# Kernel optimization log

Hardware: AMD Instinct MI355X
Metric: run time of the kernel (lower is better)

The kernel has to match this reference:

```python
import jax, jax.numpy as jnp
import numpy as np

D_MODEL = 1024
N_HEADS = 16
HEAD_DIM = D_MODEL // N_HEADS
D_FF = 4096
ROPE_BASE = 10000.0
LN_EPS = 1e-5


def setup_inputs() -> dict:
    key = jax.random.key(0)
    ks = jax.random.split(key, 12)
    B, S = 2, 2048
    s = 0.02
    inp = {
        "x": jax.random.normal(ks[0], (B, S, D_MODEL), dtype=jnp.float32),
        "Wq": jax.random.normal(ks[1], (D_MODEL, D_MODEL), dtype=jnp.float32) * s,
        "bq": jnp.zeros((D_MODEL,), jnp.float32),
        "Wk": jax.random.normal(ks[2], (D_MODEL, D_MODEL), dtype=jnp.float32) * s,
        "bk": jnp.zeros((D_MODEL,), jnp.float32),
        "Wv": jax.random.normal(ks[3], (D_MODEL, D_MODEL), dtype=jnp.float32) * s,
        "bv": jnp.zeros((D_MODEL,), jnp.float32),
        "Wo": jax.random.normal(ks[4], (D_MODEL, D_MODEL), dtype=jnp.float32) * s,
        "bo": jnp.zeros((D_MODEL,), jnp.float32),
        "ln1_g": jnp.ones((D_MODEL,), jnp.float32),
        "ln1_b": jnp.zeros((D_MODEL,), jnp.float32),
        "W1": jax.random.normal(ks[5], (D_MODEL, D_FF), dtype=jnp.float32) * s,
        "b1": jnp.zeros((D_FF,), jnp.float32),
        "W2": jax.random.normal(ks[6], (D_FF, D_MODEL), dtype=jnp.float32) * s,
        "b2": jnp.zeros((D_MODEL,), jnp.float32),
        "ln2_g": jnp.ones((D_MODEL,), jnp.float32),
        "ln2_b": jnp.zeros((D_MODEL,), jnp.float32),
    }
    return inp


def _layernorm(x, g, b):
    mu = jnp.mean(x, axis=-1, keepdims=True)
    var = jnp.var(x, axis=-1, keepdims=True)
    return (x - mu) * jax.lax.rsqrt(var + LN_EPS) * g + b


def _rope_cos_sin(seq_len, dtype):
    inv_freq = 1.0 / (ROPE_BASE ** (jnp.arange(0, HEAD_DIM, 2, dtype=jnp.float32) / HEAD_DIM))
    t = jnp.arange(seq_len, dtype=jnp.float32)
    freqs = jnp.einsum("i,j->ij", t, inv_freq)          # [S, HEAD_DIM/2]
    emb = jnp.concatenate([freqs, freqs], axis=-1)        # [S, HEAD_DIM]
    return jnp.cos(emb).astype(dtype), jnp.sin(emb).astype(dtype)


def _rotate_half(x):
    x1, x2 = jnp.split(x, 2, axis=-1)
    return jnp.concatenate([-x2, x1], axis=-1)


def reference(x, Wq, bq, Wk, bk, Wv, bv, Wo, bo, ln1_g, ln1_b,
              W1, b1, W2, b2, ln2_g, ln2_b):
    B, S, _ = x.shape
    residual = x
    h = _layernorm(x, ln1_g, ln1_b)

    def split_heads(y):  # [B,S,D] -> [B,H,S,hd]
        return y.reshape(B, S, N_HEADS, HEAD_DIM).transpose(0, 2, 1, 3)

    q = split_heads(h @ Wq + bq)
    k = split_heads(h @ Wk + bk)
    v = split_heads(h @ Wv + bv)

    cos, sin = _rope_cos_sin(S, x.dtype)  # [S, hd], broadcast over B,H
    q = q * cos + _rotate_half(q) * sin
    k = k * cos + _rotate_half(k) * sin

    scale = HEAD_DIM ** -0.5
    scores = jnp.einsum("bhqd,bhkd->bhqk", q, k) * scale
    attn = jax.nn.softmax(scores, axis=-1)
    ctx = jnp.einsum("bhqk,bhkd->bhqd", attn, v)           # [B,H,S,hd]
    ctx = ctx.transpose(0, 2, 1, 3).reshape(B, S, D_MODEL)
    attn_out = ctx @ Wo + bo

    x = residual + attn_out
    residual = x
    h = _layernorm(x, ln2_g, ln2_b)
    ffn = jax.nn.gelu(h @ W1 + b1, approximate=False) @ W2 + b2
    return residual + ffn
```

## Files before the change

### kernel.cpp

```cpp
#include <hip/hip_runtime.h>
#include <hip/hip_bf16.h>
#include <stdint.h>

#define S_LEN 2048
#define NH 16
#define HD 64
#define DM 1024
#define DFF 4096
#define MTOK 4096

typedef __attribute__((ext_vector_type(8))) short short8;
typedef __attribute__((ext_vector_type(4))) float f32x4;
typedef __attribute__((ext_vector_type(16))) float f32x16;
typedef __attribute__((ext_vector_type(2))) int i32x2;
typedef unsigned short u16;
typedef unsigned int u32;

__device__ __forceinline__ float bf2f(u16 u) {
  union { u32 i; float f; } x; x.i = ((u32)u) << 16; return x.f;
}
__device__ __forceinline__ u16 f2bf(float f) {
  union { float f; u32 i; } x; x.f = f;
  u32 r = x.i + 0x7fffu + ((x.i >> 16) & 1u);
  return (u16)(r >> 16);
}
__device__ __forceinline__ void gload16(const u16* g, u16* l) {
  __builtin_amdgcn_global_load_lds(
      (__attribute__((address_space(1))) u32*)g,
      (__attribute__((address_space(3))) u32*)l, 16, 0, 0);
}

#define VM0 asm volatile("s_waitcnt vmcnt(0)" ::: "memory")
#define VM6 asm volatile("s_waitcnt vmcnt(6)" ::: "memory")
#define BARR do { __builtin_amdgcn_s_barrier(); asm volatile("" ::: "memory"); } while (0)
#define LGKM0 do { asm volatile("s_waitcnt lgkmcnt(0)" ::: "memory"); __builtin_amdgcn_sched_barrier(0); } while (0)
#define PRIO1 __builtin_amdgcn_s_setprio(1)
#define PRIO0 __builtin_amdgcn_s_setprio(0)

__device__ __forceinline__ void transpose_tile(const float* __restrict__ W,
                                               u16* __restrict__ Wt, int K, int N,
                                               int n0, int k0, int tx, int ty,
                                               float (*tile)[33]) {
#pragma unroll
  for (int i = 0; i < 4; ++i)
    tile[ty + i * 8][tx] = W[(size_t)(k0 + ty + i * 8) * N + n0 + tx];
  __syncthreads();
#pragma unroll
  for (int i = 0; i < 4; ++i)
    Wt[(size_t)(n0 + ty + i * 8) * K + k0 + tx] = f2bf(tile[tx][ty + i * 8]);
}

__global__ __launch_bounds__(256) void prep(
    const float* __restrict__ Wq, const float* __restrict__ Wk,
    const float* __restrict__ Wv, const float* __restrict__ Wo,
    const float* __restrict__ W1, const float* __restrict__ W2,
    u16* __restrict__ WQKVT, u16* __restrict__ WOT, u16* __restrict__ W1T,
    u16* __restrict__ W2T, float* __restrict__ cosT, float* __restrict__ sinT,
    const float* __restrict__ x, const float* __restrict__ g,
    const float* __restrict__ b, u16* __restrict__ H) {
  __shared__ float tile[32][33];
  __shared__ float red[8];
  const int r = blockIdx.x;
  const int t = threadIdx.x;
  const int tx = t & 31, ty = t >> 5;
  if (r < 4096) {
    const float* W = (r < 1024) ? Wq : (r < 2048) ? Wk : (r < 3072) ? Wv : Wo;
    u16* Wt = (r < 1024) ? WQKVT
              : (r < 2048) ? WQKVT + 1024 * 1024
              : (r < 3072) ? WQKVT + 2 * 1024 * 1024 : WOT;
    int sub = r & 1023;
    transpose_tile(W, Wt, 1024, 1024, (sub & 31) * 32, (sub >> 5) * 32, tx, ty, tile);
  } else if (r < 8192) {
    int sub = r - 4096;
    transpose_tile(W1, W1T, 1024, 4096, (sub & 127) * 32, (sub >> 7) * 32, tx, ty, tile);
  } else if (r < 12288) {
    int sub = r - 8192;
    transpose_tile(W2, W2T, 4096, 1024, (sub & 31) * 32, (sub >> 5) * 32, tx, ty, tile);
  } else if (r < 12544) {
    int id = (r - 12288) * 256 + t;
    int s = id >> 5, j = id & 31;
    float inv = powf(10000.0f, -(float)j * (1.0f / 32.0f));
    float fr = (float)s * inv;
    cosT[id] = cosf(fr);
    sinT[id] = sinf(fr);
  } else {
    int row = r - 12544;
    float4 v = ((const float4*)(x + ((size_t)row << 10)))[t];
    float s = v.x + v.y + v.z + v.w;
    float q = v.x * v.x + v.y * v.y + v.z * v.z + v.w * v.w;
#pragma unroll
    for (int m = 1; m < 64; m <<= 1) {
      s += __shfl_xor(s, m, 64);
      q += __shfl_xor(q, m, 64);
    }
    int lane = t & 63, w = t >> 6;
    if (lane == 0) { red[w] = s; red[4 + w] = q; }
    __syncthreads();
    s = red[0] + red[1] + red[2] + red[3];
    q = red[4] + red[5] + red[6] + red[7];
    float mu = s * (1.0f / 1024.0f);
    float var = q * (1.0f / 1024.0f) - mu * mu;
    float rstd = rsqrtf(var + 1e-5f);
    float4 gv = ((const float4*)g)[t];
    float4 bv = ((const float4*)b)[t];
    ushort4 o;
    o.x = f2bf((v.x - mu) * rstd * gv.x + bv.x);
    o.y = f2bf((v.y - mu) * rstd * gv.y + bv.y);
    o.z = f2bf((v.z - mu) * rstd * gv.z + bv.z);
    o.w = f2bf((v.w - mu) * rstd * gv.w + bv.w);
    ((ushort4*)(H + ((size_t)row << 10)))[t] = o;
  }
}

__global__ __launch_bounds__(256) void ln_bf16(const float* __restrict__ x,
                                               const float* __restrict__ g,
                                               const float* __restrict__ b,
                                               u16* __restrict__ out) {
  int row = blockIdx.x;
  int t = threadIdx.x;
  float4 v = ((const float4*)(x + ((size_t)row << 10)))[t];
  float s = v.x + v.y + v.z + v.w;
  float q = v.x * v.x + v.y * v.y + v.z * v.z + v.w * v.w;
#pragma unroll
  for (int m = 1; m < 64; m <<= 1) {
    s += __shfl_xor(s, m, 64);
    q += __shfl_xor(q, m, 64);
  }
  __shared__ float red[8];
  int lane = t & 63, w = t >> 6;
  if (lane == 0) { red[w] = s; red[4 + w] = q; }
  __syncthreads();
  s = red[0] + red[1] + red[2] + red[3];
  q = red[4] + red[5] + red[6] + red[7];
  float mu = s * (1.0f / 1024.0f);
  float var = q * (1.0f / 1024.0f) - mu * mu;
  float rstd = rsqrtf(var + 1e-5f);
  float4 gv = ((const float4*)g)[t];
  float4 bv = ((const float4*)b)[t];
  ushort4 o;
  o.x = f2bf((v.x - mu) * rstd * gv.x + bv.x);
  o.y = f2bf((v.y - mu) * rstd * gv.y + bv.y);
  o.z = f2bf((v.z - mu) * rstd * gv.z + bv.z);
  o.w = f2bf((v.w - mu) * rstd * gv.w + bv.w);
  ((ushort4*)(out + ((size_t)row << 10)))[t] = o;
}

#define MMQ(IB, NB)                                                          \
  _Pragma("unroll") for (int i_ = 0; i_ < 4; ++i_)                           \
  _Pragma("unroll") for (int n_ = 0; n_ < 2; ++n_)                           \
  _Pragma("unroll") for (int k_ = 0; k_ < 2; ++k_)                           \
    acc[(IB) + i_][(NB) + n_] = __builtin_amdgcn_mfma_f32_16x16x32_bf16(     \
        a[i_][k_], b[(NB) + n_][k_], acc[(IB) + i_][(NB) + n_], 0, 0, 0);

template <int EPI>
__global__ __launch_bounds__(512, 2) void gemm256(
    const u16* __restrict__ A, const u16* __restrict__ Bt, int N, int K,
    const float* __restrict__ bias, const float* __restrict__ bq,
    const float* __restrict__ bk, const float* __restrict__ bv,
    const float* __restrict__ cosT, const float* __restrict__ sinT,
    u16* __restrict__ d0, u16* __restrict__ d1, u16* __restrict__ d2) {
  __shared__ __align__(16) u16 As[2][256 * 64];
  __shared__ __align__(16) u16 Bs[2][256 * 64];
  const int t = threadIdx.x;
  const int lane = t & 63, wid = t >> 6;
  const int fr = lane & 15, fq = lane >> 4;
  const int m0 = blockIdx.y << 8, n0 = blockIdx.x << 8;
  const int wmo = (wid >> 2) << 7;
  const int wno = (wid & 3) << 6;
  const int r7 = fr & 7;
  const int srow = t >> 3, ssl = t & 7;

  f32x4 acc[8][4];
#pragma unroll
  for (int i = 0; i < 8; ++i)
#pragma unroll
    for (int n = 0; n < 4; ++n) acc[i][n] = (f32x4){0.f, 0.f, 0.f, 0.f};

  short8 a[4][2], b[4][2];

  auto stageA = [&](int slot, int kt) {
#pragma unroll
    for (int c = 0; c < 4; ++c) {
      const int row = (c << 6) + srow;
      gload16(A + (size_t)(m0 + row) * K + kt + ((ssl ^ (row & 7)) << 3),
              &As[slot][(size_t)((c << 9) + t) << 3]);
    }
  };
  auto stageB = [&](int slot, int kt) {
#pragma unroll
    for (int c = 0; c < 4; ++c) {
      const int row = (c << 6) + srow;
      gload16(Bt + (size_t)(n0 + row) * K + kt + ((ssl ^ (row & 7)) << 3),
              &Bs[slot][(size_t)((c << 9) + t) << 3]);
    }
  };
  auto readA = [&](int slot, int ibase) {
#pragma unroll
    for (int i = 0; i < 4; ++i) {
      const u16* rp = &As[slot][(wmo + ((ibase + i) << 4) + fr) << 6];
      a[i][0] = *(const short8*)(rp + ((fq ^ r7) << 3));
      a[i][1] = *(const short8*)(rp + (((4 + fq) ^ r7) << 3));
    }
  };
  auto readB = [&](int slot, int nbase) {
#pragma unroll
    for (int n = 0; n < 2; ++n) {
      const u16* rp = &Bs[slot][(wno + ((nbase + n) << 4) + fr) << 6];
      b[nbase + n][0] = *(const short8*)(rp + ((fq ^ r7) << 3));
      b[nbase + n][1] = *(const short8*)(rp + (((4 + fq) ^ r7) << 3));
    }
  };

  stageA(0, 0);
  stageB(0, 0);
  const int iters = K >> 7;
  for (int it = 0; it < iters; ++it) {
    const int kt = it << 7;
    VM0; BARR;
    readA(0, 0); readB(0, 0);
    stageA(1, kt + 64);
    LGKM0; PRIO1; MMQ(0, 0); PRIO0;
    BARR;
    readB(0, 2);
    stageB(1, kt + 64);
    LGKM0; PRIO1; MMQ(0, 2); PRIO0;
    BARR;
    readA(0, 4);
    LGKM0; PRIO1; MMQ(4, 2); PRIO0;
    BARR;
    PRIO1; MMQ(4, 0); PRIO0;
    VM0; BARR;
    readA(1, 0); readB(1, 0);
    if (it + 1 < iters) stageA(0, kt + 128);
    LGKM0; PRIO1; MMQ(0, 0); PRIO0;
    BARR;
    readB(1, 2);
    if (it + 1 < iters) stageB(0, kt + 128);
    LGKM0; PRIO1; MMQ(0, 2); PRIO0;
    BARR;
    readA(1, 4);
    LGKM0; PRIO1; MMQ(4, 2); PRIO0;
    BARR;
    PRIO1; MMQ(4, 0); PRIO0;
  }

  if (EPI == 0) {
    const int colbase = n0 + wno;
    const int slice = colbase >> 10;
    const int cb = colbase & 1023;
    const int hh = cb >> 6;
    if (slice < 2) {
      const float sc = (slice == 0) ? 0.125f * 1.44269504088896f : 1.0f;
      const float* bb_ = (slice == 0) ? bq : bk;
      u16* dst = (slice == 0) ? d0 : d1;
#pragma unroll
      for (int i = 0; i < 8; ++i) {
        const int row0 = m0 + wmo + (i << 4) + (fq << 2);
#pragma unroll
        for (int n = 0; n < 2; ++n) {
          const int d = n * 16 + fr;
          const float blo = bb_[cb + d];
          const float bhi = bb_[cb + d + 32];
#pragma unroll
          for (int j = 0; j < 4; ++j) {
            const int row = row0 + j;
            const int ss = row & 2047, bb2 = row >> 11;
            const float c = cosT[ss * 32 + d];
            const float sn = sinT[ss * 32 + d];
            const float av = acc[i][n][j] + blo;
            const float bv2 = acc[i][n + 2][j] + bhi;
            const size_t base = ((size_t)((bb2 * 16 + hh) * 2048 + ss)) << 6;
            dst[base + d] = f2bf((av * c - bv2 * sn) * sc);
            dst[base + d + 32] = f2bf((bv2 * c + av * sn) * sc);
          }
        }
      }
    } else {
#pragma unroll
      for (int i = 0; i < 8; ++i) {
        const int row0 = m0 + wmo + (i << 4) + (fq << 2);
#pragma unroll
        for (int n = 0; n < 4; ++n) {
          const int d = n * 16 + fr;
          const float bia = bv[cb + d];
#pragma unroll
          for (int j = 0; j < 4; ++j) {
            const int row = row0 + j;
            const int ss = row & 2047, bb2 = row >> 11;
            d2[((size_t)((bb2 * 16 + hh) * 64 + d)) * 2048 + ss] =
                f2bf(acc[i][n][j] + bia);
          }
        }
      }
    }
  } else {
#pragma unroll
    for (int i = 0; i < 8; ++i) {
      const int row0 = m0 + wmo + (i << 4) + (fq << 2);
#pragma unroll
      for (int n = 0; n < 4; ++n) {
        const int col = n0 + wno + n * 16 + fr;
        const float bia = bias[col];
#pragma unroll
        for (int j = 0; j < 4; ++j) {
          const int row = row0 + j;
          const float v = acc[i][n][j] + bia;
          const float gl = 0.5f * v * (1.0f + erff(v * 0.70710678118f));
          d0[(size_t)row * N + col] = f2bf(gl);
        }
      }
    }
  }
}

__global__ __launch_bounds__(256, 2) void gemm_bt2(
    const u16* __restrict__ A, const u16* __restrict__ Bt, int K,
    const float* __restrict__ bias, const float* __restrict__ resid,
    float* __restrict__ dst) {
  __shared__ __align__(16) u16 As[3][128 * 64];
  __shared__ __align__(16) u16 Bs[3][64 * 64];
  const int t = threadIdx.x, lane = t & 63, wid = t >> 6;
  const int fr = lane & 15, fq = lane >> 4;
  const int bid = blockIdx.x;
  const int xcd = bid & 7, within = bid >> 3;
  const int m0 = (xcd * 4 + (within >> 4)) << 7;
  const int n0 = (within & 15) << 6;
  const int wm = (wid >> 1) << 6;
  const int wn = (wid & 1) << 5;
  const int sr = t >> 3, sl = t & 7;
  const int sw7 = fr & 7;

  f32x4 acc[4][2];
#pragma unroll
  for (int i = 0; i < 4; ++i)
#pragma unroll
    for (int n = 0; n < 2; ++n) acc[i][n] = (f32x4){0.f, 0.f, 0.f, 0.f};

  auto stage = [&](int b, int kt) {
#pragma unroll
    for (int c = 0; c < 4; ++c) {
      int R = c * 32 + sr;
      gload16(A + (size_t)(m0 + R) * K + kt + ((sl ^ (R & 7)) << 3),
              &As[b][R * 64 + sl * 8]);
    }
#pragma unroll
    for (int c = 0; c < 2; ++c) {
      int R = c * 32 + sr;
      gload16(Bt + (size_t)(n0 + R) * K + kt + ((sl ^ (R & 7)) << 3),
              &Bs[b][R * 64 + sl * 8]);
    }
  };

  stage(0, 0);
  stage(1, 64);
  const int iters = K >> 6;
  for (int it = 0; it < iters; ++it) {
    if (it + 1 < iters) { VM6; } else { VM0; }
    BARR;
    if (it + 2 < iters) stage((it + 2) % 3, (it + 2) << 6);
    const int slot = it % 3;
    short8 a[4][2], b[2][2];
#pragma unroll
    for (int i = 0; i < 4; ++i) {
      const char* rp = (const char*)&As[slot][(wm + i * 16 + fr) * 64];
      a[i][0] = *(const short8*)(rp + ((fq ^ sw7) << 4));
      a[i][1] = *(const short8*)(rp + (((4 + fq) ^ sw7) << 4));
    }
#pragma unroll
    for (int n = 0; n < 2; ++n) {
      const char* rp = (const char*)&Bs[slot][(wn + n * 16 + fr) * 64];
      b[n][0] = *(const short8*)(rp + ((fq ^ sw7) << 4));
      b[n][1] = *(const short8*)(rp + (((4 + fq) ^ sw7) << 4));
    }
    PRIO1;
#pragma unroll
    for (int i = 0; i < 4; ++i)
#pragma unroll
      for (int n = 0; n < 2; ++n)
#pragma unroll
        for (int k2 = 0; k2 < 2; ++k2)
          acc[i][n] = __builtin_amdgcn_mfma_f32_16x16x32_bf16(a[i][k2], b[n][k2],
                                                              acc[i][n], 0, 0, 0);
    PRIO0;
  }

#pragma unroll
  for (int i = 0; i < 4; ++i) {
    int row0 = m0 + wm + i * 16 + (fq << 2);
#pragma unroll
    for (int n = 0; n < 2; ++n) {
      int col = n0 + wn + n * 16 + fr;
      float bia = bias[col];
#pragma unroll
      for (int j = 0; j < 4; ++j) {
        size_t idx = (size_t)(row0 + j) * 1024 + col;
        dst[idx] = acc[i][n][j] + bia + resid[idx];
      }
    }
  }
}

__global__ __launch_bounds__(256, 4) void attn_fwd(const u16* __restrict__ q,
                                                   const u16* __restrict__ k,
                                                   const u16* __restrict__ vt,
                                                   u16* __restrict__ ctx) {
  __shared__ __align__(16) u16 Ks[2][64 * 64];
  __shared__ __align__(16) u16 Vs[2][64 * 64];
  __shared__ float Lr[4][32];
  const int t = threadIdx.x, lane = t & 63, w = t >> 6;
  const int ql = lane & 31;
  const int h = lane >> 5;
  const int bid = blockIdx.x;
  const int bh = (bid & 7) * 4 + ((bid >> 3) & 3);
  const int qt = bid >> 5;
  const int q0w = qt * 128 + w * 32;
  const size_t hbase = (size_t)bh << 17;
  const u16* kg = k + hbase;
  const u16* vg = vt + hbase;
  const int sr = t >> 3;
  const int sl = t & 7;
  const int l7 = lane & 7;

  short8 qf[4];
#pragma unroll
  for (int f = 0; f < 4; ++f)
    qf[f] = *(const short8*)(q + hbase + (size_t)(q0w + ql) * 64 + f * 16 + h * 8);

  float lacc = 0.f;
  f32x16 o[2];
#pragma unroll
  for (int db = 0; db < 2; ++db)
#pragma unroll
    for (int r = 0; r < 16; ++r) o[db][r] = 0.f;

  auto stage = [&](int buf, int kt) {
#pragma unroll
    for (int c = 0; c < 2; ++c) {
      int R = c * 32 + sr;
      int gs = sl ^ (R & 7);
      gload16(kg + (size_t)(kt + R) * 64 + gs * 8, &Ks[buf][R * 64 + sl * 8]);
    }
#pragma unroll
    for (int c = 0; c < 2; ++c) {
      int R = c * 32 + sr;
      int gs = sl ^ (R & 7);
      gload16(vg + (size_t)R * 2048 + kt + gs * 8, &Vs[buf][R * 64 + sl * 8]);
    }
  };

  stage(0, 0);
  int buf = 0;
  for (int it = 0; it < 32; ++it) {
    VM0;
    BARR;
    if (it < 31) stage(buf ^ 1, (it + 1) * 64);

    f32x16 s[2];
    PRIO1;
#pragma unroll
    for (int kb = 0; kb < 2; ++kb) {
#pragma unroll
      for (int r = 0; r < 16; ++r) s[kb][r] = 0.f;
#pragma unroll
      for (int f = 0; f < 4; ++f) {
        const u16* kr = &Ks[buf][(kb * 32 + ql) * 64 + (((2 * f + h) ^ l7) << 3)];
        s[kb] = __builtin_amdgcn_mfma_f32_32x32x16_bf16(*(const short8*)kr, qf[f],
                                                        s[kb], 0, 0, 0);
      }
    }
    PRIO0;

    float p[2][16];
#pragma unroll
    for (int kb = 0; kb < 2; ++kb)
#pragma unroll
      for (int r = 0; r < 16; ++r) {
        p[kb][r] = exp2f(s[kb][r]);
        lacc += p[kb][r];
      }

    short8 pf[4];
#pragma unroll
    for (int kb = 0; kb < 2; ++kb)
#pragma unroll
      for (int rrp = 0; rrp < 2; ++rrp) {
        u32 y0, y1, x0, x1;
        asm volatile("v_cvt_pk_bf16_f32 %0, %1, %2" : "=v"(y0)
                     : "v"(p[kb][8 * rrp + 0]), "v"(p[kb][8 * rrp + 1]));
        asm volatile("v_cvt_pk_bf16_f32 %0, %1, %2" : "=v"(y1)
                     : "v"(p[kb][8 * rrp + 2]), "v"(p[kb][8 * rrp + 3]));
        asm volatile("v_cvt_pk_bf16_f32 %0, %1, %2" : "=v"(x0)
                     : "v"(p[kb][8 * rrp + 4]), "v"(p[kb][8 * rrp + 5]));
        asm volatile("v_cvt_pk_bf16_f32 %0, %1, %2" : "=v"(x1)
                     : "v"(p[kb][8 * rrp + 6]), "v"(p[kb][8 * rrp + 7]));
        i32x2 r0 = __builtin_amdgcn_permlane32_swap((int)x0, (int)y0, false, false);
        i32x2 r1 = __builtin_amdgcn_permlane32_swap((int)x1, (int)y1, false, false);
        u32 dw[4] = {(u32)r0[1], (u32)r1[1], (u32)r0[0], (u32)r1[0]};
        pf[kb * 2 + rrp] = *(short8*)dw;
      }

    PRIO1;
#pragma unroll
    for (int db = 0; db < 2; ++db) {
#pragma unroll
      for (int f = 0; f < 4; ++f) {
        const u16* vr = &Vs[buf][(db * 32 + ql) * 64 + (((2 * f + h) ^ l7) << 3)];
        o[db] = __builtin_amdgcn_mfma_f32_32x32x16_bf16(pf[f], *(const short8*)vr,
                                                        o[db], 0, 0, 0);
      }
    }
    PRIO0;
    buf ^= 1;
  }

  lacc += __shfl_xor(lacc, 32, 64);
  Lr[w][ql] = 1.0f / lacc;
  LGKM0;

  const int bb = bh >> 4, hh = bh & 15;
#pragma unroll
  for (int r = 0; r < 16; ++r) {
    const int qr = (r & 3) + 8 * (r >> 2) + 4 * h;
    const float rl = Lr[w][qr];
    const int row = q0w + qr;
    const size_t base = (((size_t)(bb * 2048 + row)) << 10) + hh * 64;
#pragma unroll
    for (int db = 0; db < 2; ++db)
      ctx[base + db * 32 + ql] = f2bf(o[db][r] * rl);
  }
}

extern "C" void kernel_launch(void* const* d_in, const int* in_sizes, int n_in,
                              void* d_out, int out_size, void* d_ws, size_t ws_size,
                              hipStream_t stream) {
  const float* x    = (const float*)d_in[0];
  const float* Wq   = (const float*)d_in[1];
  const float* bq   = (const float*)d_in[2];
  const float* Wk   = (const float*)d_in[3];
  const float* bk   = (const float*)d_in[4];
  const float* Wv   = (const float*)d_in[5];
  const float* bv   = (const float*)d_in[6];
  const float* Wo   = (const float*)d_in[7];
  const float* bo   = (const float*)d_in[8];
  const float* ln1g = (const float*)d_in[9];
  const float* ln1b = (const float*)d_in[10];
  const float* W1   = (const float*)d_in[11];
  const float* b1   = (const float*)d_in[12];
  const float* W2   = (const float*)d_in[13];
  const float* b2   = (const float*)d_in[14];
  const float* ln2g = (const float*)d_in[15];
  const float* ln2b = (const float*)d_in[16];

  char* ws = (char*)d_ws;
  size_t off = 0;
  auto alloc = [&](size_t bytes) {
    char* p = ws + off;
    off += (bytes + 1023) & ~(size_t)1023;
    return p;
  };
  u16* WQKVT = (u16*)alloc((size_t)3 * DM * DM * 2);
  u16* WOT = (u16*)alloc((size_t)DM * DM * 2);
  u16* W1T = (u16*)alloc((size_t)DFF * DM * 2);
  u16* W2T = (u16*)alloc((size_t)DM * DFF * 2);
  float* COS = (float*)alloc((size_t)S_LEN * 32 * 4);
  float* SIN = (float*)alloc((size_t)S_LEN * 32 * 4);
  u16* H   = (u16*)alloc((size_t)MTOK * DM * 2);
  u16* Qb  = (u16*)alloc((size_t)MTOK * DM * 2);
  u16* Kb  = (u16*)alloc((size_t)MTOK * DM * 2);
  u16* VT  = (u16*)alloc((size_t)MTOK * DM * 2);
  u16* CTX = (u16*)alloc((size_t)MTOK * DM * 2);
  float* X2 = (float*)alloc((size_t)MTOK * DM * 4);
  u16* FFN1 = Qb;
  if (ws_size < off) return;

  dim3 blk256(256);
  prep<<<dim3(16640), blk256, 0, stream>>>(Wq, Wk, Wv, Wo, W1, W2, WQKVT, WOT,
                                           W1T, W2T, COS, SIN, x, ln1g, ln1b, H);
  gemm256<0><<<dim3(12, 16), dim3(512), 0, stream>>>(
      H, WQKVT, 3072, 1024, nullptr, bq, bk, bv, COS, SIN, Qb, Kb, VT);
  attn_fwd<<<dim3(512), blk256, 0, stream>>>(Qb, Kb, VT, CTX);
  gemm_bt2<<<dim3(512), blk256, 0, stream>>>(CTX, WOT, 1024, bo, x, X2);
  ln_bf16<<<4096, blk256, 0, stream>>>(X2, ln2g, ln2b, H);
  gemm256<1><<<dim3(16, 16), dim3(512), 0, stream>>>(
      H, W1T, 4096, 1024, b1, nullptr, nullptr, nullptr, nullptr, nullptr,
      FFN1, nullptr, nullptr);
  gemm_bt2<<<dim3(512), blk256, 0, stream>>>(FFN1, W2T, 4096, b2, X2, (float*)d_out);
}
```

Before: 246.1 us.

## Split attention KV range across two wave groups and merge partial outputs in LDS

New measurement: 241.6 us. Within noise of the previous version (-1.8%).

```diff
diff --git a/kernel.cpp b/kernel.cpp
--- a/kernel.cpp
+++ b/kernel.cpp
@@ -400,24 +400,25 @@
   }
 }
 
-__global__ __launch_bounds__(256, 4) void attn_fwd(const u16* __restrict__ q,
+__global__ __launch_bounds__(512, 4) void attn_fwd(const u16* __restrict__ q,
                                                    const u16* __restrict__ k,
                                                    const u16* __restrict__ vt,
                                                    u16* __restrict__ ctx) {
-  __shared__ __align__(16) u16 Ks[2][64 * 64];
-  __shared__ __align__(16) u16 Vs[2][64 * 64];
+  __shared__ __align__(16) u16 Ks[2][2][64 * 64];
+  __shared__ __align__(16) u16 Vs[2][2][64 * 64];
   __shared__ float Lr[4][32];
   const int t = threadIdx.x, lane = t & 63, w = t >> 6;
+  const int qsub = w & 3, half = w >> 2;
   const int ql = lane & 31;
   const int h = lane >> 5;
   const int bid = blockIdx.x;
   const int bh = (bid & 7) * 4 + ((bid >> 3) & 3);
   const int qt = bid >> 5;
-  const int q0w = qt * 128 + w * 32;
+  const int q0w = qt * 128 + qsub * 32;
   const size_t hbase = (size_t)bh << 17;
   const u16* kg = k + hbase;
   const u16* vg = vt + hbase;
-  const int sr = t >> 3;
+  const int srow = t >> 3;
   const int sl = t & 7;
   const int l7 = lane & 7;
 
@@ -433,27 +434,22 @@
 #pragma unroll
     for (int r = 0; r < 16; ++r) o[db][r] = 0.f;
 
-  auto stage = [&](int buf, int kt) {
-#pragma unroll
-    for (int c = 0; c < 2; ++c) {
-      int R = c * 32 + sr;
-      int gs = sl ^ (R & 7);
-      gload16(kg + (size_t)(kt + R) * 64 + gs * 8, &Ks[buf][R * 64 + sl * 8]);
-    }
-#pragma unroll
-    for (int c = 0; c < 2; ++c) {
-      int R = c * 32 + sr;
-      int gs = sl ^ (R & 7);
-      gload16(vg + (size_t)R * 2048 + kt + gs * 8, &Vs[buf][R * 64 + sl * 8]);
-    }
+  auto stage = [&](int buf, int it1) {
+    const int kt0 = it1 << 6;
+    const int kt1 = (16 + it1) << 6;
+    const int gs = sl ^ (srow & 7);
+    gload16(kg + (size_t)(kt0 + srow) * 64 + gs * 8, &Ks[0][buf][srow * 64 + sl * 8]);
+    gload16(kg + (size_t)(kt1 + srow) * 64 + gs * 8, &Ks[1][buf][srow * 64 + sl * 8]);
+    gload16(vg + (size_t)srow * 2048 + kt0 + gs * 8, &Vs[0][buf][srow * 64 + sl * 8]);
+    gload16(vg + (size_t)srow * 2048 + kt1 + gs * 8, &Vs[1][buf][srow * 64 + sl * 8]);
   };
 
   stage(0, 0);
   int buf = 0;
-  for (int it = 0; it < 32; ++it) {
+  for (int it = 0; it < 16; ++it) {
     VM0;
     BARR;
-    if (it < 31) stage(buf ^ 1, (it + 1) * 64);
+    if (it < 15) stage(buf ^ 1, it + 1);
 
     f32x16 s[2];
     PRIO1;
@@ -463,7 +459,7 @@
       for (int r = 0; r < 16; ++r) s[kb][r] = 0.f;
 #pragma unroll
       for (int f = 0; f < 4; ++f) {
-        const u16* kr = &Ks[buf][(kb * 32 + ql) * 64 + (((2 * f + h) ^ l7) << 3)];
+        const u16* kr = &Ks[half][buf][(kb * 32 + ql) * 64 + (((2 * f + h) ^ l7) << 3)];
         s[kb] = __builtin_amdgcn_mfma_f32_32x32x16_bf16(*(const short8*)kr, qf[f],
                                                         s[kb], 0, 0, 0);
       }
@@ -504,7 +500,7 @@
     for (int db = 0; db < 2; ++db) {
 #pragma unroll
       for (int f = 0; f < 4; ++f) {
-        const u16* vr = &Vs[buf][(db * 32 + ql) * 64 + (((2 * f + h) ^ l7) << 3)];
+        const u16* vr = &Vs[half][buf][(db * 32 + ql) * 64 + (((2 * f + h) ^ l7) << 3)];
         o[db] = __builtin_amdgcn_mfma_f32_32x32x16_bf16(pf[f], *(const short8*)vr,
                                                         o[db], 0, 0, 0);
       }
@@ -514,19 +510,44 @@
   }
 
   lacc += __shfl_xor(lacc, 32, 64);
-  Lr[w][ql] = 1.0f / lacc;
+
+  BARR;
+  float* mO = (float*)&Ks[0][0][0];
+  float* mL = (float*)&Vs[0][0][0];
+  if (half == 1) {
+#pragma unroll
+    for (int r = 0; r < 16; ++r) {
+      const int qr = (r & 3) + 8 * (r >> 2) + 4 * h;
+#pragma unroll
+      for (int db = 0; db < 2; ++db)
+        mO[(qsub * 32 + qr) * 64 + db * 32 + ql] = o[db][r];
+    }
+    if (h == 0) mL[qsub * 32 + ql] = lacc;
+  }
   LGKM0;
-
-  const int bb = bh >> 4, hh = bh & 15;
-#pragma unroll
-  for (int r = 0; r < 16; ++r) {
-    const int qr = (r & 3) + 8 * (r >> 2) + 4 * h;
-    const float rl = Lr[w][qr];
-    const int row = q0w + qr;
-    const size_t base = (((size_t)(bb * 2048 + row)) << 10) + hh * 64;
-#pragma unroll
-    for (int db = 0; db < 2; ++db)
-      ctx[base + db * 32 + ql] = f2bf(o[db][r] * rl);
+  BARR;
+  if (half == 0) {
+    float lsum = lacc + mL[qsub * 32 + ql];
+    Lr[qsub][ql] = 1.0f / lsum;
+#pragma unroll
+    for (int r = 0; r < 16; ++r) {
+      const int qr = (r & 3) + 8 * (r >> 2) + 4 * h;
+#pragma unroll
+      for (int db = 0; db < 2; ++db)
+        o[db][r] += mO[(qsub * 32 + qr) * 64 + db * 32 + ql];
+    }
+    LGKM0;
+    const int bb = bh >> 4, hh = bh & 15;
+#pragma unroll
+    for (int r = 0; r < 16; ++r) {
+      const int qr = (r & 3) + 8 * (r >> 2) + 4 * h;
+      const float rl = Lr[qsub][qr];
+      const int row = q0w + qr;
+      const size_t base = (((size_t)(bb * 2048 + row)) << 10) + hh * 64;
+#pragma unroll
+      for (int db = 0; db < 2; ++db)
+        ctx[base + db * 32 + ql] = f2bf(o[db][r] * rl);
+    }
   }
 }
 
@@ -578,7 +599,7 @@
                                            W1T, W2T, COS, SIN, x, ln1g, ln1b, H);
   gemm256<0><<<dim3(12, 16), dim3(512), 0, stream>>>(
       H, WQKVT, 3072, 1024, nullptr, bq, bk, bv, COS, SIN, Qb, Kb, VT);
-  attn_fwd<<<dim3(512), blk256, 0, stream>>>(Qb, Kb, VT, CTX);
+  attn_fwd<<<dim3(512), dim3(512), 0, stream>>>(Qb, Kb, VT, CTX);
   gemm_bt2<<<dim3(512), blk256, 0, stream>>>(CTX, WOT, 1024, bo, x, X2);
   ln_bf16<<<4096, blk256, 0, stream>>>(X2, ln2g, ln2b, H);
   gemm256<1><<<dim3(16, 16), dim3(512), 0, stream>>>(
```
